# Kernel tuning notes

Measured on AMD Instinct MI355X. Metric: run time of the kernel, lower is better.

Reference implementation:

```python
import jax, jax.numpy as jnp
import numpy as np

B, S, H, I = 2, 2048, 4096, 16384
EPS = 1e-12


def setup_inputs() -> dict:
    key = jax.random.key(0)
    ks = jax.random.split(key, 8)
    w_scale = 0.02
    return {
        "input": jax.random.normal(ks[0], (B, S, H), jnp.float32),
        "residual": jax.random.normal(ks[1], (B, S, H), jnp.float32),
        "bias": jax.random.normal(ks[2], (H,), jnp.float32) * w_scale,
        "attn_nw": jnp.ones((H,), jnp.float32),
        "attn_nb": jnp.zeros((H,), jnp.float32),
        "inter_w": jax.random.normal(ks[3], (I, H), jnp.float32) * w_scale,
        "inter_b": jax.random.normal(ks[4], (I,), jnp.float32) * w_scale,
        "output_w": jax.random.normal(ks[5], (H, I), jnp.float32) * w_scale,
        "output_b": jax.random.normal(ks[6], (H,), jnp.float32) * w_scale,
    }


def reference(input, residual, bias, attn_nw, attn_nb, inter_w, inter_b, output_w, output_b):
    # Fused mlp_gemm: residual_add = input + residual + attn-output bias
    residual_add = input + residual + bias  # [B,S,H]
    # LayerNorm over hidden dim with attn_nw/attn_nb
    mean = jnp.mean(residual_add, axis=-1, keepdims=True)
    var = jnp.var(residual_add, axis=-1, keepdims=True)
    ln = (residual_add - mean) * jax.lax.rsqrt(var + EPS) * attn_nw + attn_nb
    # Intermediate GEMM + bias + GELU (DeepSpeed uses tanh-approx gelu)
    inter = jax.nn.gelu(jnp.einsum("bsh,ih->bsi", ln, inter_w) + inter_b, approximate=True)
    # Output projection (vector_matmul)
    out = jnp.einsum("bsi,hi->bsh", inter, output_w)
    # bias_residual: add residual_add and output bias
    return out + residual_add + output_b
```

## Files before the change

### kernel.cpp

```cpp
#include <hip/hip_runtime.h>
#include <hip/hip_bf16.h>
#include <cstdint>
#include <math.h>

#define BM 128
#define BN 128
#define BK 64

typedef __attribute__((ext_vector_type(4))) float f32x4;
typedef __attribute__((ext_vector_type(8))) __bf16 bf16x8;

__device__ __forceinline__ unsigned short f2bf(float f) {
    union { float f; unsigned u; } v; v.f = f;
    unsigned u = v.u + 0x7fffu + ((v.u >> 16) & 1u);
    return (unsigned short)(u >> 16);
}

__device__ __forceinline__ float gelu_tanh(float x) {
    float x3 = x * x * x;
    float t = tanhf(0.7978845608028654f * (x + 0.044715f * x3));
    return 0.5f * x * (1.0f + t);
}

__device__ __forceinline__ void gload_lds16(const void* g, void* l) {
    __builtin_amdgcn_global_load_lds(
        (__attribute__((address_space(1))) void*)(uintptr_t)g,
        (__attribute__((address_space(3))) void*)(unsigned)(uintptr_t)l,
        16, 0, 0);
}

__global__ __launch_bounds__(256)
void fused_add_ln(const float* __restrict__ in, const float* __restrict__ res,
                  const float* __restrict__ bias, const float* __restrict__ nw,
                  const float* __restrict__ nb, float* __restrict__ resadd,
                  unsigned short* __restrict__ lnout, int H) {
    const int row = blockIdx.x;
    const int tid = threadIdx.x;
    const size_t base = (size_t)row * H;
    float v[16];
    float s = 0.f, ss = 0.f;
#pragma unroll
    for (int i = 0; i < 4; ++i) {
        int idx = (i * 256 + tid) * 4;
        float4 a = *(const float4*)(in + base + idx);
        float4 b = *(const float4*)(res + base + idx);
        float4 c = *(const float4*)(bias + idx);
        float x0 = a.x + b.x + c.x, x1 = a.y + b.y + c.y;
        float x2 = a.z + b.z + c.z, x3 = a.w + b.w + c.w;
        v[i * 4 + 0] = x0; v[i * 4 + 1] = x1; v[i * 4 + 2] = x2; v[i * 4 + 3] = x3;
        s += x0 + x1 + x2 + x3;
        ss += x0 * x0 + x1 * x1 + x2 * x2 + x3 * x3;
    }
#pragma unroll
    for (int off = 32; off > 0; off >>= 1) {
        s += __shfl_down(s, off);
        ss += __shfl_down(ss, off);
    }
    __shared__ float red[8];
    const int w = tid >> 6;
    if ((tid & 63) == 0) { red[w] = s; red[4 + w] = ss; }
    __syncthreads();
    s = red[0] + red[1] + red[2] + red[3];
    ss = red[4] + red[5] + red[6] + red[7];
    const float mean = s / H;
    const float var = ss / H - mean * mean;
    const float rstd = rsqrtf(var + 1e-12f);
#pragma unroll
    for (int i = 0; i < 4; ++i) {
        int idx = (i * 256 + tid) * 4;
        float4 wv = *(const float4*)(nw + idx);
        float4 bv = *(const float4*)(nb + idx);
        float4 r;
        r.x = v[i * 4 + 0]; r.y = v[i * 4 + 1]; r.z = v[i * 4 + 2]; r.w = v[i * 4 + 3];
        *(float4*)(resadd + base + idx) = r;
        ushort4 o;
        o.x = f2bf((r.x - mean) * rstd * wv.x + bv.x);
        o.y = f2bf((r.y - mean) * rstd * wv.y + bv.y);
        o.z = f2bf((r.z - mean) * rstd * wv.z + bv.z);
        o.w = f2bf((r.w - mean) * rstd * wv.w + bv.w);
        *(ushort4*)(lnout + base + idx) = o;
    }
}

__global__ __launch_bounds__(256)
void cast_w(const float* __restrict__ w, unsigned short* __restrict__ o, long long n4) {
    long long i = (long long)blockIdx.x * 256 + threadIdx.x;
    if (i >= n4) return;
    float4 f = *(const float4*)(w + i * 4);
    ushort4 u;
    u.x = f2bf(f.x); u.y = f2bf(f.y); u.z = f2bf(f.z); u.w = f2bf(f.w);
    *(ushort4*)(o + i * 4) = u;
}

template <int EPI>
__global__ __launch_bounds__(256, 2)
void gemm_bt(const unsigned short* __restrict__ A,
             const unsigned short* __restrict__ B,
             const float* __restrict__ bias_n,
             const float* __restrict__ resadd,
             void* __restrict__ Cout,
             int M, int N, int K) {
    __shared__ unsigned short sA[BM * BK];
    __shared__ unsigned short sB[BN * BK];
    const int tid = threadIdx.x;
    const int lane = tid & 63;
    const int w = tid >> 6;
    const int wr = w >> 1;
    const int wc = w & 1;
    const int nbx = N / BN;
    const int brow = blockIdx.x / nbx;
    const int bcol = blockIdx.x % nbx;

    f32x4 acc[4][4] = {};

    const int o_lin = tid * 16;
    int st_row[4], st_col[4];
#pragma unroll
    for (int i = 0; i < 4; ++i) {
        int o = i * 4096 + o_lin;
        int r = o >> 7;
        int c = (o & 127) ^ ((r & 7) << 4);
        st_row[i] = r;
        st_col[i] = c >> 1;
    }
    const unsigned short* Ag = A + (size_t)(brow * BM) * K;
    const unsigned short* Bg = B + (size_t)(bcol * BN) * K;

    for (int kt = 0; kt < K; kt += BK) {
#pragma unroll
        for (int i = 0; i < 4; ++i)
            gload_lds16(Ag + (size_t)st_row[i] * K + kt + st_col[i],
                        (char*)sA + i * 4096 + o_lin);
#pragma unroll
        for (int i = 0; i < 4; ++i)
            gload_lds16(Bg + (size_t)st_row[i] * K + kt + st_col[i],
                        (char*)sB + i * 4096 + o_lin);
        __syncthreads();

#pragma unroll
        for (int kk = 0; kk < 2; ++kk) {
            bf16x8 af[4], bfr[4];
#pragma unroll
            for (int mi = 0; mi < 4; ++mi) {
                int r = wr * 64 + mi * 16 + (lane & 15);
                int cb = (kk * 64 + (lane >> 4) * 16) ^ ((r & 7) << 4);
                af[mi] = *(const bf16x8*)((const char*)sA + r * 128 + cb);
            }
#pragma unroll
            for (int ni = 0; ni < 4; ++ni) {
                int r = wc * 64 + ni * 16 + (lane & 15);
                int cb = (kk * 64 + (lane >> 4) * 16) ^ ((r & 7) << 4);
                bfr[ni] = *(const bf16x8*)((const char*)sB + r * 128 + cb);
            }
#pragma unroll
            for (int mi = 0; mi < 4; ++mi)
#pragma unroll
                for (int ni = 0; ni < 4; ++ni)
                    acc[mi][ni] = __builtin_amdgcn_mfma_f32_16x16x32_bf16(
                        af[mi], bfr[ni], acc[mi][ni], 0, 0, 0);
        }
        __syncthreads();
    }

    const int c0 = bcol * BN + wc * 64 + (lane & 15);
    const int r0 = brow * BM + wr * 64 + (lane >> 4) * 4;
#pragma unroll
    for (int mi = 0; mi < 4; ++mi) {
#pragma unroll
        for (int j = 0; j < 4; ++j) {
            const int row = r0 + mi * 16 + j;
#pragma unroll
            for (int ni = 0; ni < 4; ++ni) {
                const int col = c0 + ni * 16;
                float x = acc[mi][ni][j] + bias_n[col];
                if (EPI == 0) {
                    ((unsigned short*)Cout)[(size_t)row * N + col] = f2bf(gelu_tanh(x));
                } else {
                    const size_t off = (size_t)row * N + col;
                    ((float*)Cout)[off] = x + resadd[off];
                }
            }
        }
    }
}

extern "C" void kernel_launch(void* const* d_in, const int* in_sizes, int n_in,
                              void* d_out, int out_size, void* d_ws, size_t ws_size,
                              hipStream_t stream) {
    const float* input    = (const float*)d_in[0];
    const float* residual = (const float*)d_in[1];
    const float* bias     = (const float*)d_in[2];
    const float* attn_nw  = (const float*)d_in[3];
    const float* attn_nb  = (const float*)d_in[4];
    const float* inter_w  = (const float*)d_in[5];
    const float* inter_b  = (const float*)d_in[6];
    const float* output_w = (const float*)d_in[7];
    const float* output_b = (const float*)d_in[8];

    const int H = in_sizes[3];
    const int I = in_sizes[6];
    const int T = in_sizes[0] / H;

    char* ws = (char*)d_ws;
    float* resadd      = (float*)ws;
    unsigned short* ln = (unsigned short*)(ws + (size_t)T * H * 4);
    unsigned short* w1 = (unsigned short*)((char*)ln + (size_t)T * H * 2);
    unsigned short* w2 = w1 + (size_t)I * H;
    unsigned short* act = w2 + (size_t)H * I;

    fused_add_ln<<<T, 256, 0, stream>>>(input, residual, bias, attn_nw, attn_nb,
                                        resadd, ln, H);

    {
        long long n4 = (long long)I * H / 4;
        int blocks = (int)((n4 + 255) / 256);
        cast_w<<<blocks, 256, 0, stream>>>(inter_w, w1, n4);
        cast_w<<<blocks, 256, 0, stream>>>(output_w, w2, n4);
    }

    {
        dim3 grid((T / BM) * (I / BN));
        gemm_bt<0><<<grid, 256, 0, stream>>>(ln, w1, inter_b, nullptr, act, T, I, H);
    }

    {
        dim3 grid((T / BM) * (H / BN));
        gemm_bt<1><<<grid, 256, 0, stream>>>(act, w2, output_b, resadd, d_out, T, H, I);
    }
}
```

Before: 1.225 ms.

## Replace GEMM with 256x256 tile, 512-thread, double-buffered LDS pipeline

Replaces the 128x128 single-buffered bf16 GEMM with a 256x256 tile kernel using 512 threads, double-buffered LDS filled by direct global-to-LDS loads, and a partial vmcnt wait so the next K-tile's loads overlap the current tile's MFMAs. It also remaps block IDs in groups of eight for L2 locality and raises wave priority around the MFMA bursts. The goal is more data reuse per loaded byte and hiding global-memory latency. In exchange it uses 128KB of LDS per block, which likely allows only one block per CU despite the launch bound, and the larger tiles reduce the grid size for the N=4096 GEMM.

```diff
diff --git a/kernel.cpp b/kernel.cpp
--- a/kernel.cpp
+++ b/kernel.cpp
@@ -2,10 +2,6 @@
 #include <hip/hip_bf16.h>
 #include <cstdint>
 #include <math.h>
-
-#define BM 128
-#define BN 128
-#define BK 64
 
 typedef __attribute__((ext_vector_type(4))) float f32x4;
 typedef __attribute__((ext_vector_type(8))) __bf16 bf16x8;
@@ -92,80 +88,111 @@
     *(ushort4*)(o + i * 4) = u;
 }
 
+#define GBM 256
+#define GBN 256
+#define GBK 64
+
 template <int EPI>
-__global__ __launch_bounds__(256, 2)
-void gemm_bt(const unsigned short* __restrict__ A,
+__global__ __launch_bounds__(512, 2)
+void gemm256(const unsigned short* __restrict__ A,
              const unsigned short* __restrict__ B,
              const float* __restrict__ bias_n,
              const float* __restrict__ resadd,
              void* __restrict__ Cout,
              int M, int N, int K) {
-    __shared__ unsigned short sA[BM * BK];
-    __shared__ unsigned short sB[BN * BK];
+    __shared__ unsigned short lds[2][2][GBM * GBK];
     const int tid = threadIdx.x;
     const int lane = tid & 63;
     const int w = tid >> 6;
-    const int wr = w >> 1;
-    const int wc = w & 1;
-    const int nbx = N / BN;
-    const int brow = blockIdx.x / nbx;
-    const int bcol = blockIdx.x % nbx;
-
-    f32x4 acc[4][4] = {};
-
-    const int o_lin = tid * 16;
-    int st_row[4], st_col[4];
-#pragma unroll
-    for (int i = 0; i < 4; ++i) {
-        int o = i * 4096 + o_lin;
-        int r = o >> 7;
-        int c = (o & 127) ^ ((r & 7) << 4);
-        st_row[i] = r;
-        st_col[i] = c >> 1;
-    }
-    const unsigned short* Ag = A + (size_t)(brow * BM) * K;
-    const unsigned short* Bg = B + (size_t)(bcol * BN) * K;
-
-    for (int kt = 0; kt < K; kt += BK) {
-#pragma unroll
-        for (int i = 0; i < 4; ++i)
-            gload_lds16(Ag + (size_t)st_row[i] * K + kt + st_col[i],
-                        (char*)sA + i * 4096 + o_lin);
-#pragma unroll
-        for (int i = 0; i < 4; ++i)
-            gload_lds16(Bg + (size_t)st_row[i] * K + kt + st_col[i],
-                        (char*)sB + i * 4096 + o_lin);
-        __syncthreads();
-
-#pragma unroll
-        for (int kk = 0; kk < 2; ++kk) {
-            bf16x8 af[4], bfr[4];
-#pragma unroll
-            for (int mi = 0; mi < 4; ++mi) {
-                int r = wr * 64 + mi * 16 + (lane & 15);
-                int cb = (kk * 64 + (lane >> 4) * 16) ^ ((r & 7) << 4);
-                af[mi] = *(const bf16x8*)((const char*)sA + r * 128 + cb);
+    const int wr = w >> 2;
+    const int wc = w & 3;
+
+    const int nwg = gridDim.x;
+    const int lg = (blockIdx.x & 7) * (nwg >> 3) + (blockIdx.x >> 3);
+    const int nbx = N / GBN;
+    const int brow = lg / nbx;
+    const int bcol = lg % nbx;
+
+    const int srow = tid >> 3;
+    const int scol = ((((tid & 7) << 4) ^ ((srow & 7) << 4)) >> 1);
+    const unsigned short* srcA = A + (size_t)(brow * GBM + srow) * K + scol;
+    const unsigned short* srcB = B + (size_t)(bcol * GBN + srow) * K + scol;
+    char* ldsBase = (char*)&lds[0][0][0];
+    const int dOff = tid * 16;
+
+    f32x4 acc[8][4] = {};
+
+    const int NT = K / GBK;
+    int cur = 0;
+
+#pragma unroll
+    for (int c = 0; c < 4; ++c) {
+        gload_lds16(srcA + (size_t)(c * 64) * K, ldsBase + c * 8192 + dOff);
+        gload_lds16(srcB + (size_t)(c * 64) * K, ldsBase + 32768 + c * 8192 + dOff);
+    }
+
+    const int lrow = lane & 15;
+    const int lswz = (lane & 7) << 4;
+    const int lkx = (lane >> 4) << 4;
+
+    for (int t = 0; t < NT; ++t) {
+        if (t + 1 < NT) {
+            const int kt = (t + 1) * GBK;
+            char* dst = ldsBase + (cur ^ 1) * 65536;
+#pragma unroll
+            for (int c = 0; c < 4; ++c) {
+                gload_lds16(srcA + (size_t)(c * 64) * K + kt, dst + c * 8192 + dOff);
+                gload_lds16(srcB + (size_t)(c * 64) * K + kt, dst + 32768 + c * 8192 + dOff);
             }
-#pragma unroll
-            for (int ni = 0; ni < 4; ++ni) {
-                int r = wc * 64 + ni * 16 + (lane & 15);
-                int cb = (kk * 64 + (lane >> 4) * 16) ^ ((r & 7) << 4);
-                bfr[ni] = *(const bf16x8*)((const char*)sB + r * 128 + cb);
+            asm volatile("s_waitcnt vmcnt(8)" ::: "memory");
+        } else {
+            asm volatile("s_waitcnt vmcnt(0)" ::: "memory");
+        }
+        __builtin_amdgcn_s_barrier();
+        __builtin_amdgcn_sched_barrier(0);
+
+        const char* sA = (const char*)ldsBase + cur * 65536;
+        const char* sB = sA + 32768;
+        bf16x8 bq[4][2];
+#pragma unroll
+        for (int q = 0; q < 4; ++q) {
+            if (q == 0) {
+#pragma unroll
+                for (int ni = 0; ni < 4; ++ni)
+#pragma unroll
+                    for (int kk = 0; kk < 2; ++kk)
+                        bq[ni][kk] = *(const bf16x8*)(sB
+                            + ((wc * 64 + ni * 16 + lrow) << 7)
+                            + (((kk << 6) | lkx) ^ lswz));
             }
-#pragma unroll
-            for (int mi = 0; mi < 4; ++mi)
+            bf16x8 aq[2][2];
+#pragma unroll
+            for (int m2 = 0; m2 < 2; ++m2)
+#pragma unroll
+                for (int kk = 0; kk < 2; ++kk)
+                    aq[m2][kk] = *(const bf16x8*)(sA
+                        + ((wr * 128 + (q * 2 + m2) * 16 + lrow) << 7)
+                        + (((kk << 6) | lkx) ^ lswz));
+            __builtin_amdgcn_s_setprio(1);
+#pragma unroll
+            for (int m2 = 0; m2 < 2; ++m2)
 #pragma unroll
                 for (int ni = 0; ni < 4; ++ni)
-                    acc[mi][ni] = __builtin_amdgcn_mfma_f32_16x16x32_bf16(
-                        af[mi], bfr[ni], acc[mi][ni], 0, 0, 0);
+#pragma unroll
+                    for (int kk = 0; kk < 2; ++kk)
+                        acc[q * 2 + m2][ni] = __builtin_amdgcn_mfma_f32_16x16x32_bf16(
+                            aq[m2][kk], bq[ni][kk], acc[q * 2 + m2][ni], 0, 0, 0);
+            __builtin_amdgcn_s_setprio(0);
         }
-        __syncthreads();
-    }
-
-    const int c0 = bcol * BN + wc * 64 + (lane & 15);
-    const int r0 = brow * BM + wr * 64 + (lane >> 4) * 4;
-#pragma unroll
-    for (int mi = 0; mi < 4; ++mi) {
+        __builtin_amdgcn_sched_barrier(0);
+        __builtin_amdgcn_s_barrier();
+        cur ^= 1;
+    }
+
+    const int c0 = bcol * GBN + wc * 64 + lrow;
+    const int r0 = brow * GBM + wr * 128 + (lane >> 4) * 4;
+#pragma unroll
+    for (int mi = 0; mi < 8; ++mi) {
 #pragma unroll
         for (int j = 0; j < 4; ++j) {
             const int row = r0 + mi * 16 + j;
@@ -219,12 +246,12 @@
     }
 
     {
-        dim3 grid((T / BM) * (I / BN));
-        gemm_bt<0><<<grid, 256, 0, stream>>>(ln, w1, inter_b, nullptr, act, T, I, H);
+        dim3 grid((T / GBM) * (I / GBN));
+        gemm256<0><<<grid, 512, 0, stream>>>(ln, w1, inter_b, nullptr, act, T, I, H);
     }
 
     {
-        dim3 grid((T / BM) * (H / BN));
-        gemm_bt<1><<<grid, 256, 0, stream>>>(act, w2, output_b, resadd, d_out, T, H, I);
-    }
-}
+        dim3 grid((T / GBM) * (H / GBN));
+        gemm256<1><<<grid, 512, 0, stream>>>(act, w2, output_b, resadd, d_out, T, H, I);
+    }
+}
```

Measured after the change: 1.262 ms. +3.0%, slower.
